# Kernel optimization log

Hardware: AMD Instinct MI355X
Metric: run time of the kernel (lower is better)

## Reference

```python
import jax, jax.numpy as jnp
import numpy as np

D_MODEL = 1024
NHEAD = 16
HEAD_DIM = D_MODEL // NHEAD
WINDOW = 33  # mask keeps |i-j| > WINDOW//2 (True = attend, matching torch SDPA bool-mask semantics)


def setup_inputs() -> dict:
    key = jax.random.key(0)
    ks = jax.random.split(key, 9)
    s = 1.0 / np.sqrt(D_MODEL)
    x = jax.random.normal(ks[0], (2, 2048, D_MODEL), dtype=jnp.float32)
    Wq = jax.random.uniform(ks[1], (D_MODEL, D_MODEL), jnp.float32, -s, s)
    bq = jax.random.uniform(ks[2], (D_MODEL,), jnp.float32, -s, s)
    Wk = jax.random.uniform(ks[3], (D_MODEL, D_MODEL), jnp.float32, -s, s)
    bk = jax.random.uniform(ks[4], (D_MODEL,), jnp.float32, -s, s)
    Wv = jax.random.uniform(ks[5], (D_MODEL, D_MODEL), jnp.float32, -s, s)
    bv = jax.random.uniform(ks[6], (D_MODEL,), jnp.float32, -s, s)
    Wo = jax.random.uniform(ks[7], (D_MODEL, D_MODEL), jnp.float32, -s, s)
    bo = jax.random.uniform(ks[8], (D_MODEL,), jnp.float32, -s, s)
    return {"x": x, "Wq": Wq, "bq": bq, "Wk": Wk, "bk": bk,
            "Wv": Wv, "bv": bv, "Wo": Wo, "bo": bo}


def reference(x, Wq, bq, Wk, bk, Wv, bv, Wo, bo):
    B, T, C = x.shape
    H, D = NHEAD, HEAD_DIM
    # projections (torch Linear: y = x @ W.T + b)
    q = (x @ Wq.T + bq).reshape(B, T, H, D).transpose(0, 2, 1, 3)  # [B,H,T,D]
    k = (x @ Wk.T + bk).reshape(B, T, H, D).transpose(0, 2, 1, 3)
    v = (x @ Wv.T + bv).reshape(B, T, H, D).transpose(0, 2, 1, 3)
    idx = jnp.arange(T)
    rel = jnp.abs(idx[:, None] - idx[None, :])
    keep = rel > (WINDOW // 2)  # True = participate (torch SDPA bool-mask semantics)
    scale = 1.0 / jnp.sqrt(jnp.asarray(D, dtype=x.dtype))
    scores = jnp.einsum('bhqd,bhkd->bhqk', q, k) * scale
    scores = jnp.where(keep, scores, jnp.asarray(-jnp.inf, dtype=scores.dtype))
    attn = jax.nn.softmax(scores, axis=-1)
    out = jnp.einsum('bhqk,bhkd->bhqd', attn, v)  # [B,H,T,D]
    out = out.transpose(0, 2, 1, 3).reshape(B, T, C)
    return out @ Wo.T + bo
```

## Files before the change

### kernel.cpp

```cpp
#include <hip/hip_runtime.h>
#include <stdint.h>


typedef unsigned short u16;
typedef short bf16x8 __attribute__((ext_vector_type(8)));
typedef float f32x4 __attribute__((ext_vector_type(4)));

#define MFMA16 __builtin_amdgcn_mfma_f32_16x16x32_bf16

__device__ __forceinline__ u16 f2bf(float f) {
  union { float f; uint32_t u; } v; v.f = f;
  return (u16)((v.u + 0x7fffu + ((v.u >> 16) & 1u)) >> 16);
}

__device__ __forceinline__ uint32_t cvt_pk_bf16(float lo, float hi) {
  uint32_t d;
  asm("v_cvt_pk_bf16_f32 %0, %1, %2" : "=v"(d) : "v"(lo), "v"(hi));
  return d;
}

__device__ __forceinline__ void gload_lds16(const void* g, void* l) {
  __builtin_amdgcn_global_load_lds(
      (const __attribute__((address_space(1))) unsigned int*)g,
      (__attribute__((address_space(3))) unsigned int*)l, 16, 0, 0);
}

__global__ void f2b_kernel(const float* __restrict__ in, u16* __restrict__ out, int n4) {
  int i = blockIdx.x * blockDim.x + threadIdx.x;
  if (i < n4) {
    float4 v = reinterpret_cast<const float4*>(in)[i];
    ushort4 o;
    o.x = f2bf(v.x); o.y = f2bf(v.y); o.z = f2bf(v.z); o.w = f2bf(v.w);
    reinterpret_cast<ushort4*>(out)[i] = o;
  }
}

__global__ void f2b4_kernel(const float* __restrict__ a, const float* __restrict__ b,
                            const float* __restrict__ c, const float* __restrict__ d,
                            u16* __restrict__ oa, u16* __restrict__ ob,
                            u16* __restrict__ oc, u16* __restrict__ od, int n4) {
  int i = blockIdx.x * blockDim.x + threadIdx.x;
  if (i >= n4) return;
  int w = blockIdx.y;
  const float* src = (w == 0) ? a : (w == 1) ? b : (w == 2) ? c : d;
  u16* dst = (w == 0) ? oa : (w == 1) ? ob : (w == 2) ? oc : od;
  float4 v = reinterpret_cast<const float4*>(src)[i];
  ushort4 o;
  o.x = f2bf(v.x); o.y = f2bf(v.y); o.z = f2bf(v.z); o.w = f2bf(v.w);
  reinterpret_cast<ushort4*>(dst)[i] = o;
}

__global__ __launch_bounds__(256) void gemm_qkv(
    const u16* __restrict__ A,
    const u16* __restrict__ Wqb, const u16* __restrict__ Wkb, const u16* __restrict__ Wvb,
    const float* __restrict__ bqp, const float* __restrict__ bkp, const float* __restrict__ bvp,
    u16* __restrict__ qo, u16* __restrict__ ko, u16* __restrict__ vo)
{
  constexpr int K = 1024;
  __shared__ __align__(16) u16 As[128 * 64];
  __shared__ __align__(16) u16 Bs[128 * 64];

  const int bid = blockIdx.x + gridDim.x * blockIdx.y;
  const int sid = (bid & 7) * 96 + (bid >> 3);
  const int bm0 = (sid / 24) * 128;
  const int jy = sid % 24;
  const int sel = jy >> 3;
  const int bn0 = (jy & 7) * 128;

  const u16* Bw = (sel == 0) ? Wqb : (sel == 1) ? Wkb : Wvb;
  const float* bias = (sel == 0) ? bqp : (sel == 1) ? bkp : bvp;
  const float scale = (sel == 0) ? 0.125f : 1.0f;

  const int t = threadIdx.x;
  const int lane = t & 63;
  const int wv = t >> 6;
  const int wm = (wv >> 1) * 64;
  const int wn = (wv & 1) * 64;
  const int lg = lane >> 4;
  const int lr = lane & 15;

  f32x4 acc[4][4];
  for (int i = 0; i < 4; ++i)
    for (int j = 0; j < 4; ++j) acc[i][j] = (f32x4)0.0f;

  for (int k0 = 0; k0 < K; k0 += 64) {
    for (int it = 0; it < 4; ++it) {
      int chunk = it * 256 + t;
      int row = chunk >> 3;
      int col = (chunk & 7) * 8;
      int base = (it * 256 + wv * 64) * 8;
      gload_lds16(A  + (size_t)(bm0 + row) * K + k0 + col, &As[base]);
      gload_lds16(Bw + (size_t)(bn0 + row) * K + k0 + col, &Bs[base]);
    }
    __syncthreads();
    for (int kk = 0; kk < 2; ++kk) {
      bf16x8 af[4], bfr[4];
      for (int i = 0; i < 4; ++i)
        af[i] = *reinterpret_cast<const bf16x8*>(&As[(wm + i * 16 + lr) * 64 + kk * 32 + lg * 8]);
      for (int j = 0; j < 4; ++j)
        bfr[j] = *reinterpret_cast<const bf16x8*>(&Bs[(wn + j * 16 + lr) * 64 + kk * 32 + lg * 8]);
      for (int i = 0; i < 4; ++i)
        for (int j = 0; j < 4; ++j)
          acc[i][j] = MFMA16(af[i], bfr[j], acc[i][j], 0, 0, 0);
    }
    __syncthreads();
  }

  for (int j = 0; j < 4; ++j) {
    int gn = bn0 + wn + j * 16 + lr;
    float bv = bias[gn];
    for (int i = 0; i < 4; ++i) {
      for (int r = 0; r < 4; ++r) {
        int gm = bm0 + wm + i * 16 + lg * 4 + r;
        float val = (acc[i][j][r] + bv) * scale;
        int b = gm >> 11, tt = gm & 2047;
        int h = gn >> 6,  d = gn & 63;
        u16 o = f2bf(val);
        if (sel == 0)
          qo[((size_t)(b * 16 + h) * 2048 + tt) * 64 + d] = o;
        else if (sel == 1)
          ko[((size_t)(b * 16 + h) * 2048 + tt) * 64 + d] = o;
        else
          vo[((size_t)(b * 16 + h) * 64 + d) * 2048 + tt] = o;
      }
    }
  }
}

__global__ __launch_bounds__(256) void gemm_out(
    const u16* __restrict__ A, const u16* __restrict__ Bw,
    const float* __restrict__ bias, float* __restrict__ outp)
{
  constexpr int K = 1024;
  __shared__ __align__(16) u16 As[128 * 64];
  __shared__ __align__(16) u16 Bs[128 * 64];
  const int t = threadIdx.x;
  const int lane = t & 63;
  const int wv = t >> 6;
  const int bm0 = blockIdx.x * 128;
  const int bn0 = blockIdx.y * 128;
  const int wm = (wv >> 1) * 64;
  const int wn = (wv & 1) * 64;
  const int lg = lane >> 4;
  const int lr = lane & 15;

  f32x4 acc[4][4];
  for (int i = 0; i < 4; ++i)
    for (int j = 0; j < 4; ++j) acc[i][j] = (f32x4)0.0f;

  for (int k0 = 0; k0 < K; k0 += 64) {
    for (int it = 0; it < 4; ++it) {
      int chunk = it * 256 + t;
      int row = chunk >> 3;
      int col = (chunk & 7) * 8;
      int base = (it * 256 + wv * 64) * 8;
      gload_lds16(A  + (size_t)(bm0 + row) * K + k0 + col, &As[base]);
      gload_lds16(Bw + (size_t)(bn0 + row) * K + k0 + col, &Bs[base]);
    }
    __syncthreads();
    for (int kk = 0; kk < 2; ++kk) {
      bf16x8 af[4], bfr[4];
      for (int i = 0; i < 4; ++i)
        af[i] = *reinterpret_cast<const bf16x8*>(&As[(wm + i * 16 + lr) * 64 + kk * 32 + lg * 8]);
      for (int j = 0; j < 4; ++j)
        bfr[j] = *reinterpret_cast<const bf16x8*>(&Bs[(wn + j * 16 + lr) * 64 + kk * 32 + lg * 8]);
      for (int i = 0; i < 4; ++i)
        for (int j = 0; j < 4; ++j)
          acc[i][j] = MFMA16(af[i], bfr[j], acc[i][j], 0, 0, 0);
    }
    __syncthreads();
  }

  for (int j = 0; j < 4; ++j) {
    int gn = bn0 + wn + j * 16 + lr;
    float bv = bias[gn];
    for (int i = 0; i < 4; ++i)
      for (int r = 0; r < 4; ++r) {
        int gm = bm0 + wm + i * 16 + lg * 4 + r;
        outp[(size_t)gm * 1024 + gn] = acc[i][j][r] + bv;
      }
  }
}

__global__ __launch_bounds__(256, 2) void attn_kernel(
    const u16* __restrict__ qb, const u16* __restrict__ kb,
    const u16* __restrict__ vtb, u16* __restrict__ ab)
{
  constexpr int KP = 72;
  __shared__ __align__(16) u16 Kb[2][64 * KP];
  __shared__ __align__(16) u16 Vb[2][64 * KP];
  __shared__ __align__(16) u16 Pl[4][32 * 64];

  const int bid = blockIdx.x + gridDim.x * blockIdx.y;
  const int sid = (bid & 7) * 64 + (bid >> 3);
  const int bx = sid & 15;
  const int bh = sid >> 4;

  const int t = threadIdx.x;
  const int lane = t & 63;
  const int wv = t >> 6;
  const int lg = lane >> 4, lr = lane & 15;
  const int q0 = bx * 128 + wv * 32;

  const u16* Qp = qb + (size_t)bh * 2048 * 64;
  const u16* Kp = kb + (size_t)bh * 2048 * 64;
  const u16* Vt = vtb + (size_t)bh * 64 * 2048;
  char* Pw = (char*)&Pl[wv][0];
  const int swz = (lr & 7) << 4;

  const int sl = lane & 7;
  const int r0 = wv * 16 + (lane >> 3);
  const int sdst0 = r0 * (KP * 2) + sl * 16;

  uint4 krA, krB, vrA, vrB;

#define ISSUE_LOADS(J0N)                                                                 \
  do {                                                                                   \
    krA = *reinterpret_cast<const uint4*>(Kp + (size_t)((J0N) + r0) * 64 + sl * 8);      \
    krB = *reinterpret_cast<const uint4*>(Kp + (size_t)((J0N) + r0 + 8) * 64 + sl * 8);  \
    vrA = *reinterpret_cast<const uint4*>(Vt + (size_t)r0 * 2048 + (J0N) + sl * 8);      \
    vrB = *reinterpret_cast<const uint4*>(Vt + (size_t)(r0 + 8) * 2048 + (J0N) + sl * 8);\
  } while (0)

#define WRITE_LDS(BUF)                                                                   \
  do {                                                                                   \
    *reinterpret_cast<uint4*>((char*)&Kb[BUF][0] + sdst0)                = krA;          \
    *reinterpret_cast<uint4*>((char*)&Kb[BUF][0] + sdst0 + 8 * KP * 2)   = krB;          \
    *reinterpret_cast<uint4*>((char*)&Vb[BUF][0] + sdst0)                = vrA;          \
    *reinterpret_cast<uint4*>((char*)&Vb[BUF][0] + sdst0 + 8 * KP * 2)   = vrB;          \
  } while (0)

  bf16x8 qf[2][2];
  for (int qi = 0; qi < 2; ++qi)
    for (int h = 0; h < 2; ++h)
      qf[qi][h] = *reinterpret_cast<const bf16x8*>(&Qp[(size_t)(q0 + qi * 16 + lr) * 64 + h * 32 + lg * 8]);

  f32x4 o[2][4];
  for (int qi = 0; qi < 2; ++qi)
    for (int d = 0; d < 4; ++d) o[qi][d] = (f32x4)0.0f;
  float m[2] = {-1e30f, -1e30f};
  float l[2] = {0.0f, 0.0f};

  ISSUE_LOADS(0);
  WRITE_LDS(0);
  __syncthreads();
  int cur = 0;

  for (int tt = 0; tt < 32; ++tt) {
    if (tt < 31) ISSUE_LOADS((tt + 1) * 64);
    const int j0 = tt * 64;

    f32x4 s[2][4];
    for (int kc = 0; kc < 4; ++kc) {
      bf16x8 kf0 = *reinterpret_cast<const bf16x8*>(&Kb[cur][(kc * 16 + lr) * KP + lg * 8]);
      bf16x8 kf1 = *reinterpret_cast<const bf16x8*>(&Kb[cur][(kc * 16 + lr) * KP + 32 + lg * 8]);
      for (int qi = 0; qi < 2; ++qi) {
        f32x4 z = (f32x4)0.0f;
        z = MFMA16(kf0, qf[qi][0], z, 0, 0, 0);
        z = MFMA16(kf1, qf[qi][1], z, 0, 0, 0);
        s[qi][kc] = z;
      }
    }
    if (j0 + 63 >= q0 - 16 && j0 <= q0 + 47) {
      for (int qi = 0; qi < 2; ++qi)
        for (int kc = 0; kc < 4; ++kc)
          for (int r = 0; r < 4; ++r) {
            int i = q0 + qi * 16 + lr;
            int j = j0 + kc * 16 + lg * 4 + r;
            int dd = i - j; if (dd < 0) dd = -dd;
            if (dd <= 16) s[qi][kc][r] = -1e38f;
          }
    }
    float pm[2];
    for (int qi = 0; qi < 2; ++qi) {
      f32x4 t4 = s[qi][0];
      t4 = __builtin_elementwise_max(t4, s[qi][1]);
      t4 = __builtin_elementwise_max(t4, s[qi][2]);
      t4 = __builtin_elementwise_max(t4, s[qi][3]);
      float x = fmaxf(fmaxf(t4[0], t4[1]), fmaxf(t4[2], t4[3]));
      x = fmaxf(x, __shfl_xor(x, 16));
      x = fmaxf(x, __shfl_xor(x, 32));
      pm[qi] = x;
    }
    bool need = (pm[0] > m[0] + 8.0f) || (pm[1] > m[1] + 8.0f);
    if (__any((int)need)) {
      for (int qi = 0; qi < 2; ++qi) {
        float mn = fmaxf(m[qi], pm[qi]);
        float a = __expf(m[qi] - mn);
        m[qi] = mn;
        l[qi] *= a;
        for (int d = 0; d < 4; ++d) o[qi][d] *= a;
      }
    }
    for (int qi = 0; qi < 2; ++qi) {
      float sum = 0.0f;
      int rowbase = (qi * 16 + lr) * 128;
      for (int kc = 0; kc < 4; ++kc) {
        float p0 = __expf(s[qi][kc][0] - m[qi]);
        float p1 = __expf(s[qi][kc][1] - m[qi]);
        float p2 = __expf(s[qi][kc][2] - m[qi]);
        float p3 = __expf(s[qi][kc][3] - m[qi]);
        sum += (p0 + p1) + (p2 + p3);
        uint2 pk;
        pk.x = cvt_pk_bf16(p0, p1);
        pk.y = cvt_pk_bf16(p2, p3);
        *reinterpret_cast<uint2*>(Pw + ((rowbase + kc * 32 + lg * 8) ^ swz)) = pk;
      }
      sum += __shfl_xor(sum, 16);
      sum += __shfl_xor(sum, 32);
      l[qi] += sum;
    }
    asm volatile("s_waitcnt lgkmcnt(0)" ::: "memory");
    for (int kh = 0; kh < 2; ++kh) {
      bf16x8 pa[2];
      for (int qi = 0; qi < 2; ++qi)
        pa[qi] = *reinterpret_cast<const bf16x8*>(
            Pw + (((qi * 16 + lr) * 128 + kh * 64 + lg * 16) ^ swz));
      for (int d = 0; d < 4; ++d) {
        bf16x8 vf = *reinterpret_cast<const bf16x8*>(
            &Vb[cur][(d * 16 + lr) * KP + kh * 32 + lg * 8]);
        for (int qi = 0; qi < 2; ++qi)
          o[qi][d] = MFMA16(vf, pa[qi], o[qi][d], 0, 0, 0);
      }
    }
    if (tt < 31) WRITE_LDS(cur ^ 1);
    __syncthreads();
    cur ^= 1;
  }

  int b = bh >> 4, h = bh & 15;
  for (int qi = 0; qi < 2; ++qi) {
    float inv = 1.0f / l[qi];
    size_t rowoff = ((size_t)b * 2048 + q0 + qi * 16 + lr) * 1024 + h * 64;
    for (int d = 0; d < 4; ++d) {
      uint2 pk;
      pk.x = cvt_pk_bf16(o[qi][d][0] * inv, o[qi][d][1] * inv);
      pk.y = cvt_pk_bf16(o[qi][d][2] * inv, o[qi][d][3] * inv);
      *reinterpret_cast<uint2*>(&ab[rowoff + d * 16 + lg * 4]) = pk;
    }
  }
#undef ISSUE_LOADS
#undef WRITE_LDS
}

extern "C" void kernel_launch(void* const* d_in, const int* in_sizes, int n_in,
                              void* d_out, int out_size, void* d_ws, size_t ws_size,
                              hipStream_t stream) {
  const float* x  = (const float*)d_in[0];
  const float* Wq = (const float*)d_in[1];
  const float* bq = (const float*)d_in[2];
  const float* Wk = (const float*)d_in[3];
  const float* bk = (const float*)d_in[4];
  const float* Wv = (const float*)d_in[5];
  const float* bv = (const float*)d_in[6];
  const float* Wo = (const float*)d_in[7];
  const float* bo = (const float*)d_in[8];

  u16* ws  = (u16*)d_ws;
  u16* xb  = ws;
  u16* wqb = ws + 4194304;
  u16* wkb = ws + 5242880;
  u16* wvb = ws + 6291456;
  u16* wob = ws + 7340032;
  u16* qbf = ws + 8388608;
  u16* kbf = ws + 12582912;
  u16* vbf = ws + 16777216;
  u16* ab  = xb;

  f2b_kernel<<<4096, 256, 0, stream>>>(x, xb, 1048576);
  f2b4_kernel<<<dim3(1024, 4), 256, 0, stream>>>(Wq, Wk, Wv, Wo, wqb, wkb, wvb, wob, 262144);

  gemm_qkv<<<dim3(32, 24), 256, 0, stream>>>(xb, wqb, wkb, wvb, bq, bk, bv, qbf, kbf, vbf);

  attn_kernel<<<dim3(16, 32), 256, 0, stream>>>(qbf, kbf, vbf, ab);

  gemm_out<<<dim3(32, 8), 256, 0, stream>>>(ab, wob, bo, (float*)d_out);
}
```

Before: 167.1 us.

## Register-prefetch GEMM tiles with padded LDS rows instead of direct global-to-LDS loads

Both projection GEMMs now load the next K-tile from global memory into registers while MFMAs run on the current LDS tile, then store it to LDS at the top of the next iteration. The LDS rows are padded to 72 elements to avoid bank conflicts on the fragment reads. The earlier unpadded rows with 16-byte fragment reads may have caused conflicts. This replaces the synchronous global_load_lds path, overlapping load latency with compute at the cost of extra VGPRs and explicit LDS stores.

Result: slower. 246.0 us (+47.2%).

```diff
diff --git a/kernel.cpp b/kernel.cpp
--- a/kernel.cpp
+++ b/kernel.cpp
@@ -17,12 +17,6 @@
   uint32_t d;
   asm("v_cvt_pk_bf16_f32 %0, %1, %2" : "=v"(d) : "v"(lo), "v"(hi));
   return d;
-}
-
-__device__ __forceinline__ void gload_lds16(const void* g, void* l) {
-  __builtin_amdgcn_global_load_lds(
-      (const __attribute__((address_space(1))) unsigned int*)g,
-      (__attribute__((address_space(3))) unsigned int*)l, 16, 0, 0);
 }
 
 __global__ void f2b_kernel(const float* __restrict__ in, u16* __restrict__ out, int n4) {
@@ -50,16 +44,59 @@
   reinterpret_cast<ushort4*>(dst)[i] = o;
 }
 
+#define GEMM_CORE(A_, B_, bm0_, bn0_)                                                     \
+  constexpr int K = 1024;                                                                 \
+  constexpr int KP = 72;                                                                  \
+  __shared__ __align__(16) u16 As[128 * KP];                                              \
+  __shared__ __align__(16) u16 Bs[128 * KP];                                              \
+  const int t = threadIdx.x;                                                              \
+  const int lane = t & 63;                                                                \
+  const int wv = t >> 6;                                                                  \
+  const int wm = (wv >> 1) * 64;                                                          \
+  const int wn = (wv & 1) * 64;                                                           \
+  const int lg = lane >> 4;                                                               \
+  const int lr = lane & 15;                                                               \
+  const int srow = t >> 3;                      \
+  const int sslot = t & 7;                                   \
+  uint4 ar[4], br[4];                                                                     \
+  f32x4 acc[4][4];                                                                        \
+  for (int i = 0; i < 4; ++i)                                                             \
+    for (int j = 0; j < 4; ++j) acc[i][j] = (f32x4)0.0f;                                  \
+  for (int it = 0; it < 4; ++it) {                                                        \
+    ar[it] = *reinterpret_cast<const uint4*>(A_ + (size_t)(bm0_ + it * 32 + srow) * K + sslot * 8); \
+    br[it] = *reinterpret_cast<const uint4*>(B_ + (size_t)(bn0_ + it * 32 + srow) * K + sslot * 8); \
+  }                                                                                       \
+  for (int k0 = 0; k0 < K; k0 += 64) {                                                    \
+    for (int it = 0; it < 4; ++it) {                                                      \
+      *reinterpret_cast<uint4*>((char*)As + (it * 32 + srow) * 144 + sslot * 16) = ar[it];\
+      *reinterpret_cast<uint4*>((char*)Bs + (it * 32 + srow) * 144 + sslot * 16) = br[it];\
+    }                                                                                     \
+    __syncthreads();                                                                      \
+    if (k0 + 64 < K) {                                                                    \
+      for (int it = 0; it < 4; ++it) {                                                    \
+        ar[it] = *reinterpret_cast<const uint4*>(A_ + (size_t)(bm0_ + it * 32 + srow) * K + k0 + 64 + sslot * 8); \
+        br[it] = *reinterpret_cast<const uint4*>(B_ + (size_t)(bn0_ + it * 32 + srow) * K + k0 + 64 + sslot * 8); \
+      }                                                                                   \
+    }                                                                                     \
+    for (int kk = 0; kk < 2; ++kk) {                                                      \
+      bf16x8 af[4], bfr[4];                                                               \
+      for (int i = 0; i < 4; ++i)                                                         \
+        af[i] = *reinterpret_cast<const bf16x8*>(&As[(wm + i * 16 + lr) * KP + kk * 32 + lg * 8]); \
+      for (int j = 0; j < 4; ++j)                                                         \
+        bfr[j] = *reinterpret_cast<const bf16x8*>(&Bs[(wn + j * 16 + lr) * KP + kk * 32 + lg * 8]); \
+      for (int i = 0; i < 4; ++i)                                                         \
+        for (int j = 0; j < 4; ++j)                                                       \
+          acc[i][j] = MFMA16(af[i], bfr[j], acc[i][j], 0, 0, 0);                          \
+    }                                                                                     \
+    __syncthreads();                                                                      \
+  }
+
 __global__ __launch_bounds__(256) void gemm_qkv(
     const u16* __restrict__ A,
     const u16* __restrict__ Wqb, const u16* __restrict__ Wkb, const u16* __restrict__ Wvb,
     const float* __restrict__ bqp, const float* __restrict__ bkp, const float* __restrict__ bvp,
     u16* __restrict__ qo, u16* __restrict__ ko, u16* __restrict__ vo)
 {
-  constexpr int K = 1024;
-  __shared__ __align__(16) u16 As[128 * 64];
-  __shared__ __align__(16) u16 Bs[128 * 64];
-
   const int bid = blockIdx.x + gridDim.x * blockIdx.y;
   const int sid = (bid & 7) * 96 + (bid >> 3);
   const int bm0 = (sid / 24) * 128;
@@ -71,40 +108,7 @@
   const float* bias = (sel == 0) ? bqp : (sel == 1) ? bkp : bvp;
   const float scale = (sel == 0) ? 0.125f : 1.0f;
 
-  const int t = threadIdx.x;
-  const int lane = t & 63;
-  const int wv = t >> 6;
-  const int wm = (wv >> 1) * 64;
-  const int wn = (wv & 1) * 64;
-  const int lg = lane >> 4;
-  const int lr = lane & 15;
-
-  f32x4 acc[4][4];
-  for (int i = 0; i < 4; ++i)
-    for (int j = 0; j < 4; ++j) acc[i][j] = (f32x4)0.0f;
-
-  for (int k0 = 0; k0 < K; k0 += 64) {
-    for (int it = 0; it < 4; ++it) {
-      int chunk = it * 256 + t;
-      int row = chunk >> 3;
-      int col = (chunk & 7) * 8;
-      int base = (it * 256 + wv * 64) * 8;
-      gload_lds16(A  + (size_t)(bm0 + row) * K + k0 + col, &As[base]);
-      gload_lds16(Bw + (size_t)(bn0 + row) * K + k0 + col, &Bs[base]);
-    }
-    __syncthreads();
-    for (int kk = 0; kk < 2; ++kk) {
-      bf16x8 af[4], bfr[4];
-      for (int i = 0; i < 4; ++i)
-        af[i] = *reinterpret_cast<const bf16x8*>(&As[(wm + i * 16 + lr) * 64 + kk * 32 + lg * 8]);
-      for (int j = 0; j < 4; ++j)
-        bfr[j] = *reinterpret_cast<const bf16x8*>(&Bs[(wn + j * 16 + lr) * 64 + kk * 32 + lg * 8]);
-      for (int i = 0; i < 4; ++i)
-        for (int j = 0; j < 4; ++j)
-          acc[i][j] = MFMA16(af[i], bfr[j], acc[i][j], 0, 0, 0);
-    }
-    __syncthreads();
-  }
+  GEMM_CORE(A, Bw, bm0, bn0)
 
   for (int j = 0; j < 4; ++j) {
     int gn = bn0 + wn + j * 16 + lr;
@@ -131,45 +135,10 @@
     const u16* __restrict__ A, const u16* __restrict__ Bw,
     const float* __restrict__ bias, float* __restrict__ outp)
 {
-  constexpr int K = 1024;
-  __shared__ __align__(16) u16 As[128 * 64];
-  __shared__ __align__(16) u16 Bs[128 * 64];
-  const int t = threadIdx.x;
-  const int lane = t & 63;
-  const int wv = t >> 6;
   const int bm0 = blockIdx.x * 128;
   const int bn0 = blockIdx.y * 128;
-  const int wm = (wv >> 1) * 64;
-  const int wn = (wv & 1) * 64;
-  const int lg = lane >> 4;
-  const int lr = lane & 15;
-
-  f32x4 acc[4][4];
-  for (int i = 0; i < 4; ++i)
-    for (int j = 0; j < 4; ++j) acc[i][j] = (f32x4)0.0f;
-
-  for (int k0 = 0; k0 < K; k0 += 64) {
-    for (int it = 0; it < 4; ++it) {
-      int chunk = it * 256 + t;
-      int row = chunk >> 3;
-      int col = (chunk & 7) * 8;
-      int base = (it * 256 + wv * 64) * 8;
-      gload_lds16(A  + (size_t)(bm0 + row) * K + k0 + col, &As[base]);
-      gload_lds16(Bw + (size_t)(bn0 + row) * K + k0 + col, &Bs[base]);
-    }
-    __syncthreads();
-    for (int kk = 0; kk < 2; ++kk) {
-      bf16x8 af[4], bfr[4];
-      for (int i = 0; i < 4; ++i)
-        af[i] = *reinterpret_cast<const bf16x8*>(&As[(wm + i * 16 + lr) * 64 + kk * 32 + lg * 8]);
-      for (int j = 0; j < 4; ++j)
-        bfr[j] = *reinterpret_cast<const bf16x8*>(&Bs[(wn + j * 16 + lr) * 64 + kk * 32 + lg * 8]);
-      for (int i = 0; i < 4; ++i)
-        for (int j = 0; j < 4; ++j)
-          acc[i][j] = MFMA16(af[i], bfr[j], acc[i][j], 0, 0, 0);
-    }
-    __syncthreads();
-  }
+
+  GEMM_CORE(A, Bw, bm0, bn0)
 
   for (int j = 0; j < 4; ++j) {
     int gn = bn0 + wn + j * 16 + lr;
```
